# Kernel tuning notes

Hardware: AMD Instinct MI355X
Metric: run time of the kernel (lower is better)

## Reference

```python
import jax, jax.numpy as jnp
import numpy as np

B, N, D, H = 2, 2048, 1024, 16
DK = D // H


def setup_inputs() -> dict:
    key = jax.random.key(0)
    ks = jax.random.split(key, 8)
    s = 1.0 / np.sqrt(D)  # keep projection outputs O(1)
    return {
        "x": jax.random.normal(ks[0], (B, N, D), jnp.float32),
        "alpha": jax.random.uniform(ks[1], (B, N), jnp.float32, -1.0, 1.0),
        "bias": jax.random.normal(ks[2], (B, N, N), jnp.float32) * 0.1,
        "Wq": jax.random.normal(ks[3], (D, D), jnp.float32) * s,
        "bq": jnp.zeros((D,), jnp.float32),
        "Wk": jax.random.normal(ks[4], (D, D), jnp.float32) * s,
        "bk": jnp.zeros((D,), jnp.float32),
        "Wv": jax.random.normal(ks[5], (D, D), jnp.float32) * s,
        "bv": jnp.zeros((D,), jnp.float32),
        "Wo": jax.random.normal(ks[6], (D, D), jnp.float32) * s,
        "bo": jnp.zeros((D,), jnp.float32),
    }


def reference(x, alpha, bias, Wq, bq, Wk, bk, Wv, bv, Wo, bo):
    b, n, d = x.shape
    # projections -> (B, H, N, DK)
    def split_heads(t):
        return t.reshape(b, n, H, DK).transpose(0, 2, 1, 3)

    q = split_heads(x @ Wq + bq)
    k = split_heads(x @ Wk + bk)
    v = split_heads(x @ Wv + bv)

    # salience rescale of keys/values: (B,1,N,1)
    scale = 1.0 + alpha[:, None, :, None]
    k = k * scale
    v = v * scale

    logits = jnp.einsum("bhnd,bhmd->bhnm", q, k) / np.float32(np.sqrt(DK))
    logits = logits + bias[:, None, :, :]  # broadcast over heads
    attn = jax.nn.softmax(logits, axis=-1)

    y = jnp.einsum("bhnm,bhmd->bhnd", attn, v)
    y = y.transpose(0, 2, 1, 3).reshape(b, n, d)
    return y @ Wo + bo
```

## Files before the change

### kernel.cpp

```cpp
#include <hip/hip_runtime.h>

typedef __attribute__((ext_vector_type(8))) short bf16x8;
typedef __attribute__((ext_vector_type(4))) float f32x4;

#define LOG2E 1.4426950408889634f

static __device__ __forceinline__ unsigned short f2bf(float f) {
    unsigned int u = __builtin_bit_cast(unsigned int, f);
    u += 0x7fffu + ((u >> 16) & 1u);
    return (unsigned short)(u >> 16);
}
static __device__ __forceinline__ float bf2f(unsigned short h) {
    unsigned int u = ((unsigned int)h) << 16;
    return __builtin_bit_cast(float, u);
}
static __device__ __forceinline__ void gload_lds16(const void* g, void* l) {
    __builtin_amdgcn_global_load_lds(
        (const __attribute__((address_space(1))) void*)g,
        (__attribute__((address_space(3))) void*)l, 16, 0, 0);
}

__global__ void convert_bf16(const float* __restrict__ src,
                             unsigned short* __restrict__ dst, int n8) {
    int i = blockIdx.x * blockDim.x + threadIdx.x;
    if (i >= n8) return;
    const float4* s4 = (const float4*)src;
    float4 a = s4[2 * i], b = s4[2 * i + 1];
    uint4 u;
    u.x = (unsigned)f2bf(a.x) | ((unsigned)f2bf(a.y) << 16);
    u.y = (unsigned)f2bf(a.z) | ((unsigned)f2bf(a.w) << 16);
    u.z = (unsigned)f2bf(b.x) | ((unsigned)f2bf(b.y) << 16);
    u.w = (unsigned)f2bf(b.z) | ((unsigned)f2bf(b.w) << 16);
    *(uint4*)(dst + 8 * (size_t)i) = u;
}

__global__ void bias_permute(const float* __restrict__ src,
                             unsigned short* __restrict__ dst) {
    int mt = blockIdx.x, qt = blockIdx.y, b = blockIdx.z;
    int tid = threadIdx.x, w = tid >> 6, lane = tid & 63;
    int quad = lane >> 4, l16 = lane & 15;
    const float* s = src + (size_t)b * 2048 * 2048;
    unsigned short* d = dst + (((size_t)(b * 16 + qt) * 32 + mt) * 8192);
    for (int e = 0; e < 2; e++) {
        unsigned short vals[16];
        for (int c = 0; c < 4; c++)
            for (int r = 0; r < 4; r++) {
                int q = qt * 128 + e * 64 + w * 16 + quad * 4 + r;
                int k = mt * 64 + c * 16 + l16;
                vals[c * 4 + r] = f2bf(s[(size_t)q * 2048 + k] * LOG2E);
            }
        unsigned short* o = d + ((size_t)((e * 4 + w) * 64 + lane)) * 16;
        *(bf16x8*)&o[0] = *(bf16x8*)&vals[0];
        *(bf16x8*)&o[8] = *(bf16x8*)&vals[8];
    }
}

__global__ void transpose_convert4(const float* __restrict__ W0,
                                   const float* __restrict__ W1,
                                   const float* __restrict__ W2,
                                   const float* __restrict__ W3,
                                   unsigned short* __restrict__ T0,
                                   unsigned short* __restrict__ T1,
                                   unsigned short* __restrict__ T2,
                                   unsigned short* __restrict__ T3) {
    const float* W = (blockIdx.z == 0) ? W0 : (blockIdx.z == 1) ? W1
                     : (blockIdx.z == 2) ? W2 : W3;
    unsigned short* Wt = (blockIdx.z == 0) ? T0 : (blockIdx.z == 1) ? T1
                         : (blockIdx.z == 2) ? T2 : T3;
    __shared__ float t[32][33];
    int tx = threadIdx.x, ty = threadIdx.y;
    int x0 = blockIdx.x * 32, y0 = blockIdx.y * 32;
    for (int i = 0; i < 4; i++)
        t[ty + 8 * i][tx] = W[(size_t)(y0 + ty + 8 * i) * 1024 + x0 + tx];
    __syncthreads();
    for (int i = 0; i < 4; i++)
        Wt[(size_t)(x0 + ty + 8 * i) * 1024 + y0 + tx] = f2bf(t[tx][ty + 8 * i]);
}

__launch_bounds__(256)
__global__ void gemm_qkv(const unsigned short* __restrict__ A,
                         const unsigned short* __restrict__ WqT,
                         const unsigned short* __restrict__ WkT,
                         const unsigned short* __restrict__ WvT,
                         const float* __restrict__ bq,
                         const float* __restrict__ bk,
                         const float* __restrict__ bv,
                         const float* __restrict__ alpha,
                         unsigned short* __restrict__ Qb,
                         unsigned short* __restrict__ Kb,
                         unsigned short* __restrict__ Vtb) {
    int which = blockIdx.y >> 3;
    const unsigned short* Bt = (which == 0) ? WqT : (which == 1) ? WkT : WvT;
    const float* bias = (which == 0) ? bq : (which == 1) ? bk : bv;

    __shared__ __align__(16) unsigned short As[128][64];
    __shared__ __align__(16) unsigned short Bs[128][64];
    int tid = threadIdx.x;
    int wave = tid >> 6, lane = tid & 63, quad = lane >> 4, l16 = lane & 15;
    int wm = wave & 1, wn = wave >> 1;
    int lrow = lane >> 3, lblk = lane & 7;
    int swz = ((lblk ^ lrow) * 8);
    int m0 = blockIdx.x * 128, n0 = (blockIdx.y & 7) * 128;
    f32x4 acc[4][4] = {};

    for (int kt = 0; kt < 16; kt++) {
        int k0 = kt * 64;
        for (int i = 0; i < 4; i++) {
            int rbase = i * 32 + wave * 8;
            gload_lds16(&A[(size_t)(m0 + rbase + lrow) * 1024 + k0 + swz],
                        &As[rbase][0]);
            gload_lds16(&Bt[(size_t)(n0 + rbase + lrow) * 1024 + k0 + swz],
                        &Bs[rbase][0]);
        }
        __syncthreads();
        for (int ks = 0; ks < 2; ks++) {
            int pblk = ((ks * 4 + quad) ^ (l16 & 7)) * 8;
            bf16x8 af[4], bf_[4];
            for (int i = 0; i < 4; i++)
                af[i] = *(const bf16x8*)&As[64 * wm + 16 * i + l16][pblk];
            for (int j = 0; j < 4; j++)
                bf_[j] = *(const bf16x8*)&Bs[64 * wn + 16 * j + l16][pblk];
            if (which == 2) {
                for (int i = 0; i < 4; i++)
                    for (int j = 0; j < 4; j++)
                        acc[i][j] = __builtin_amdgcn_mfma_f32_16x16x32_bf16(
                            af[i], bf_[j], acc[i][j], 0, 0, 0);
            } else {
                for (int i = 0; i < 4; i++)
                    for (int j = 0; j < 4; j++)
                        acc[i][j] = __builtin_amdgcn_mfma_f32_16x16x32_bf16(
                            bf_[j], af[i], acc[i][j], 0, 0, 0);
            }
        }
        __syncthreads();
    }

    if (which == 2) {
        for (int i = 0; i < 4; i++)
            for (int j = 0; j < 4; j++) {
                int colb = n0 + 64 * wn + 16 * j + l16;
                int h = colb >> 6, dk = colb & 63;
                int row0 = m0 + 64 * wm + 16 * i + quad * 4;
                int bb = row0 >> 11, nn0 = row0 & 2047;
                unsigned short v4[4];
                for (int r = 0; r < 4; r++) {
                    float v = acc[i][j][r] + bias[colb];
                    v4[r] = f2bf(v * (1.0f + alpha[bb * 2048 + nn0 + r]));
                }
                uint2 u;
                u.x = (unsigned)v4[0] | ((unsigned)v4[1] << 16);
                u.y = (unsigned)v4[2] | ((unsigned)v4[3] << 16);
                *(uint2*)&Vtb[((size_t)(bb * 16 + h) * 64 + dk) * 2048 + nn0] = u;
            }
    } else {
        unsigned short* outb = (which == 0) ? Qb : Kb;
        for (int i = 0; i < 4; i++)
            for (int j = 0; j < 4; j++) {
                int row = m0 + 64 * wm + 16 * i + l16;
                int bb = row >> 11, nn = row & 2047;
                int colb0 = n0 + 64 * wn + 16 * j + quad * 4;
                int h = colb0 >> 6, dk0 = colb0 & 63;
                float4 b4 = *(const float4*)&bias[colb0];
                float s = (which == 0) ? (0.125f * LOG2E)
                                       : (1.0f + alpha[bb * 2048 + nn]);
                unsigned short v4[4];
                v4[0] = f2bf((acc[i][j][0] + b4.x) * s);
                v4[1] = f2bf((acc[i][j][1] + b4.y) * s);
                v4[2] = f2bf((acc[i][j][2] + b4.z) * s);
                v4[3] = f2bf((acc[i][j][3] + b4.w) * s);
                uint2 u;
                u.x = (unsigned)v4[0] | ((unsigned)v4[1] << 16);
                u.y = (unsigned)v4[2] | ((unsigned)v4[3] << 16);
                *(uint2*)&outb[((size_t)(bb * 16 + h) * 2048 + nn) * 64 + dk0] = u;
            }
    }
}

__launch_bounds__(256)
__global__ void gemm_out(const unsigned short* __restrict__ A,
                         const unsigned short* __restrict__ Bt,
                         const float* __restrict__ bias,
                         float* __restrict__ outf) {
    __shared__ __align__(16) unsigned short As[128][64];
    __shared__ __align__(16) unsigned short Bs[128][64];
    int tid = threadIdx.x;
    int wave = tid >> 6, lane = tid & 63, quad = lane >> 4, l16 = lane & 15;
    int wm = wave & 1, wn = wave >> 1;
    int lrow = lane >> 3, lblk = lane & 7;
    int swz = ((lblk ^ lrow) * 8);
    int m0 = blockIdx.x * 128, n0 = blockIdx.y * 128;
    f32x4 acc[4][4] = {};

    for (int kt = 0; kt < 16; kt++) {
        int k0 = kt * 64;
        for (int i = 0; i < 4; i++) {
            int rbase = i * 32 + wave * 8;
            gload_lds16(&A[(size_t)(m0 + rbase + lrow) * 1024 + k0 + swz],
                        &As[rbase][0]);
            gload_lds16(&Bt[(size_t)(n0 + rbase + lrow) * 1024 + k0 + swz],
                        &Bs[rbase][0]);
        }
        __syncthreads();
        for (int ks = 0; ks < 2; ks++) {
            int pblk = ((ks * 4 + quad) ^ (l16 & 7)) * 8;
            bf16x8 af[4], bf_[4];
            for (int i = 0; i < 4; i++)
                af[i] = *(const bf16x8*)&As[64 * wm + 16 * i + l16][pblk];
            for (int j = 0; j < 4; j++)
                bf_[j] = *(const bf16x8*)&Bs[64 * wn + 16 * j + l16][pblk];
            for (int i = 0; i < 4; i++)
                for (int j = 0; j < 4; j++)
                    acc[i][j] = __builtin_amdgcn_mfma_f32_16x16x32_bf16(
                        bf_[j], af[i], acc[i][j], 0, 0, 0);
        }
        __syncthreads();
    }

    for (int i = 0; i < 4; i++)
        for (int j = 0; j < 4; j++) {
            int row = m0 + 64 * wm + 16 * i + l16;
            int colb0 = n0 + 64 * wn + 16 * j + quad * 4;
            float4 b4 = *(const float4*)&bias[colb0];
            float4 o;
            o.x = acc[i][j][0] + b4.x;
            o.y = acc[i][j][1] + b4.y;
            o.z = acc[i][j][2] + b4.z;
            o.w = acc[i][j][3] + b4.w;
            *(float4*)&outf[(size_t)row * 1024 + colb0] = o;
        }
}

__launch_bounds__(256, 4)
__global__ void attn_kernel(const unsigned short* __restrict__ Q,
                            const unsigned short* __restrict__ K,
                            const unsigned short* __restrict__ Vt,
                            const unsigned short* __restrict__ biasP,
                            unsigned short* __restrict__ Y,
                            float* __restrict__ Opart,
                            float* __restrict__ Lpart, int split) {
    __shared__ __align__(16) unsigned short Ks[64][64];
    __shared__ __align__(16) unsigned short Vs[64][64];
    __shared__ __align__(16) unsigned short Ps[4][32][72];
    int tid = threadIdx.x;
    int wave = tid >> 6, lane = tid & 63, quad = lane >> 4, l16 = lane & 15;
    int qt = blockIdx.x, h = blockIdx.y;
    int b, mt0, mtN;
    if (split) { b = blockIdx.z >> 1; int half = blockIdx.z & 1;
                 mt0 = half * 16; mtN = mt0 + 16; }
    else       { b = blockIdx.z; mt0 = 0; mtN = 32; }
    int q0 = qt * 128;
    size_t headoff = (size_t)(b * 16 + h) * 2048 * 64;
    const unsigned short* Kp = K + headoff;
    const unsigned short* Vp = Vt + headoff;
    int lrow = lane >> 3, lblk = lane & 7;
    int swz = (lblk ^ lrow) * 8;

    bf16x8 aq[2][2];
    for (int e = 0; e < 2; e++) {
        const unsigned short* qp =
            Q + headoff + (size_t)(q0 + e * 64 + wave * 16 + l16) * 64;
        aq[e][0] = *(const bf16x8*)&qp[quad * 8];
        aq[e][1] = *(const bf16x8*)&qp[32 + quad * 8];
    }
    bf16x8 ones;
    for (int j = 0; j < 8; j++) ones[j] = (short)0x3F80;

    f32x4 oacc[2][4] = {};
    f32x4 lacc[2] = {};
    const unsigned short* bP = biasP + (size_t)(b * 16 + qt) * 32 * 8192;

    for (int mt = mt0; mt < mtN; mt++) {
        int m0 = mt * 64;
        for (int i = 0; i < 2; i++) {
            int rbase = wave * 16 + i * 8;
            gload_lds16(&Kp[(size_t)(m0 + rbase + lrow) * 64 + swz], &Ks[rbase][0]);
            gload_lds16(&Vp[(size_t)(rbase + lrow) * 2048 + m0 + swz], &Vs[rbase][0]);
        }
        const unsigned short* bt = bP + (size_t)mt * 8192;
        bf16x8 bz[2][2];
        for (int e = 0; e < 2; e++) {
            const unsigned short* p = bt + (size_t)((e * 4 + wave) * 64 + lane) * 16;
            bz[e][0] = *(const bf16x8*)&p[0];
            bz[e][1] = *(const bf16x8*)&p[8];
        }
        __syncthreads();

        f32x4 sc[2][4];
        for (int e = 0; e < 2; e++)
            for (int c = 0; c < 4; c++) {
                f32x4 s;
                for (int r = 0; r < 4; r++)
                    s[r] = bf2f(((unsigned short*)&bz[e][c >> 1])[(c & 1) * 4 + r]);
                sc[e][c] = s;
            }
        for (int c = 0; c < 4; c++) {
            for (int ks = 0; ks < 2; ks++) {
                bf16x8 kf = *(const bf16x8*)&Ks[c * 16 + l16]
                                               [((ks * 4 + quad) ^ (l16 & 7)) * 8];
                sc[0][c] = __builtin_amdgcn_mfma_f32_16x16x32_bf16(aq[0][ks], kf, sc[0][c], 0, 0, 0);
                sc[1][c] = __builtin_amdgcn_mfma_f32_16x16x32_bf16(aq[1][ks], kf, sc[1][c], 0, 0, 0);
            }
        }

        for (int e = 0; e < 2; e++)
            for (int c = 0; c < 4; c++) {
                int colw = (((c * 2 + (l16 >> 3)) + quad) & 7) * 8 + (l16 & 7);
                for (int r = 0; r < 4; r++) {
                    float p = exp2f(sc[e][c][r]);
                    unsigned int u = __builtin_bit_cast(unsigned int, p);
                    Ps[wave][e * 16 + quad * 4 + r][colw] = (unsigned short)(u >> 16);
                }
            }

        for (int ks = 0; ks < 2; ks++) {
            int blkr = (ks * 4 + quad + (l16 >> 2)) & 7;
            bf16x8 pf0 = *(const bf16x8*)&Ps[wave][l16][blkr * 8];
            bf16x8 pf1 = *(const bf16x8*)&Ps[wave][16 + l16][blkr * 8];
            lacc[0] = __builtin_amdgcn_mfma_f32_16x16x32_bf16(pf0, ones, lacc[0], 0, 0, 0);
            lacc[1] = __builtin_amdgcn_mfma_f32_16x16x32_bf16(pf1, ones, lacc[1], 0, 0, 0);
            for (int cv = 0; cv < 4; cv++) {
                bf16x8 vf = *(const bf16x8*)&Vs[cv * 16 + l16]
                                               [((ks * 4 + quad) ^ (l16 & 7)) * 8];
                oacc[0][cv] = __builtin_amdgcn_mfma_f32_16x16x32_bf16(pf0, vf, oacc[0][cv], 0, 0, 0);
                oacc[1][cv] = __builtin_amdgcn_mfma_f32_16x16x32_bf16(pf1, vf, oacc[1][cv], 0, 0, 0);
            }
        }
        __syncthreads();
    }

    if (split) {
        size_t p = ((size_t)((b * 16 + h) * 16 + qt)) * 2 + (blockIdx.z & 1);
        float* Op = Opart + p * 8192;
        for (int e = 0; e < 2; e++)
            for (int cv = 0; cv < 4; cv++)
                for (int r = 0; r < 4; r++)
                    Op[(e * 64 + wave * 16 + quad * 4 + r) * 64 + cv * 16 + l16] =
                        oacc[e][cv][r];
        if (l16 == 0)
            for (int e = 0; e < 2; e++)
                for (int r = 0; r < 4; r++)
                    Lpart[p * 128 + e * 64 + wave * 16 + quad * 4 + r] = lacc[e][r];
    } else {
        for (int e = 0; e < 2; e++) {
            float invl[4];
            for (int r = 0; r < 4; r++) invl[r] = 1.0f / lacc[e][r];
            for (int cv = 0; cv < 4; cv++)
                for (int r = 0; r < 4; r++) {
                    int qrow = q0 + e * 64 + 16 * wave + quad * 4 + r;
                    int d = h * 64 + cv * 16 + l16;
                    Y[((size_t)b * 2048 + qrow) * 1024 + d] =
                        f2bf(oacc[e][cv][r] * invl[r]);
                }
        }
    }
}

__global__ void attn_combine(const float* __restrict__ Opart,
                             const float* __restrict__ Lpart,
                             unsigned short* __restrict__ Y) {
    int blk = blockIdx.x;
    int qt = blk & 15, h = (blk >> 4) & 15, b = blk >> 8;
    const float* O0 = Opart + (size_t)blk * 2 * 8192;
    const float* O1 = O0 + 8192;
    const float* L0 = Lpart + (size_t)blk * 2 * 128;
    const float* L1 = L0 + 128;
    int t = threadIdx.x;
    for (int i = 0; i < 8; i++) {
        int idx4 = i * 256 + t;
        int q = idx4 >> 4;
        int dk = (idx4 & 15) * 4;
        float4 a = *(const float4*)&O0[idx4 * 4];
        float4 c = *(const float4*)&O1[idx4 * 4];
        float inv = 1.0f / (L0[q] + L1[q]);
        uint2 u;
        u.x = (unsigned)f2bf((a.x + c.x) * inv) |
              ((unsigned)f2bf((a.y + c.y) * inv) << 16);
        u.y = (unsigned)f2bf((a.z + c.z) * inv) |
              ((unsigned)f2bf((a.w + c.w) * inv) << 16);
        int qrow = qt * 128 + q;
        *(uint2*)&Y[((size_t)b * 2048 + qrow) * 1024 + h * 64 + dk] = u;
    }
}

extern "C" void kernel_launch(void* const* d_in, const int* in_sizes, int n_in,
                              void* d_out, int out_size, void* d_ws, size_t ws_size,
                              hipStream_t stream) {
    const float* x     = (const float*)d_in[0];
    const float* alpha = (const float*)d_in[1];
    const float* bias  = (const float*)d_in[2];
    const float* Wq    = (const float*)d_in[3];
    const float* bq    = (const float*)d_in[4];
    const float* Wk    = (const float*)d_in[5];
    const float* bk    = (const float*)d_in[6];
    const float* Wv    = (const float*)d_in[7];
    const float* bv    = (const float*)d_in[8];
    const float* Wo    = (const float*)d_in[9];
    const float* bo    = (const float*)d_in[10];
    float* out = (float*)d_out;

    char* ws = (char*)d_ws;
    const size_t MB = 1048576;
    unsigned short* xb    = (unsigned short*)(ws);
    unsigned short* wqt   = (unsigned short*)(ws + 8 * MB);
    unsigned short* wkt   = (unsigned short*)(ws + 10 * MB);
    unsigned short* wvt   = (unsigned short*)(ws + 12 * MB);
    unsigned short* wot   = (unsigned short*)(ws + 14 * MB);
    unsigned short* Qb    = (unsigned short*)(ws + 16 * MB);
    unsigned short* Kb    = (unsigned short*)(ws + 24 * MB);
    unsigned short* Vtb   = (unsigned short*)(ws + 32 * MB);
    unsigned short* biasP = (unsigned short*)(ws + 40 * MB);
    float*          Opart = (float*)(ws + 56 * MB);
    float*          Lpart = (float*)(ws + 88 * MB);
    unsigned short* Yb    = xb;
    int split = (ws_size >= 90 * MB) ? 1 : 0;

    convert_bf16<<<2048, 256, 0, stream>>>(x, xb, 524288);
    bias_permute<<<dim3(32, 16, 2), 256, 0, stream>>>(bias, biasP);
    transpose_convert4<<<dim3(32, 32, 4), dim3(32, 8), 0, stream>>>(
        Wq, Wk, Wv, Wo, wqt, wkt, wvt, wot);

    gemm_qkv<<<dim3(32, 24), 256, 0, stream>>>(
        xb, wqt, wkt, wvt, bq, bk, bv, alpha, Qb, Kb, Vtb);

    if (split) {
        attn_kernel<<<dim3(16, 16, 4), 256, 0, stream>>>(
            Qb, Kb, Vtb, biasP, Yb, Opart, Lpart, 1);
        attn_combine<<<512, 256, 0, stream>>>(Opart, Lpart, Yb);
    } else {
        attn_kernel<<<dim3(16, 16, 2), 256, 0, stream>>>(
            Qb, Kb, Vtb, biasP, Yb, Opart, Lpart, 0);
    }

    gemm_out<<<dim3(32, 8), 256, 0, stream>>>(Yb, wot, bo, out);
}
```

Measured before the change: 251.3 us.

## Merge prep kernels into one launch, stage bias through LDS, add MFMA priority hints

Replaces the three preprocessing launches (x conversion, weight transpose, bias permute) with a single prep kernel that dispatches on block index, removing two launch overheads. The bias permute now loads coalesced float4 rows into LDS before scattering, instead of strided global reads. In the attention loop, bias unpacking uses 32-bit word shifts and masks, and s_setprio raises wave priority around the MFMA sections. The merged kernel allocates 34KB of shared memory for every block, including x-conversion blocks that do not use it, which may lower occupancy for those blocks.

```diff
diff --git a/kernel.cpp b/kernel.cpp
--- a/kernel.cpp
+++ b/kernel.cpp
@@ -10,71 +10,80 @@
     u += 0x7fffu + ((u >> 16) & 1u);
     return (unsigned short)(u >> 16);
 }
-static __device__ __forceinline__ float bf2f(unsigned short h) {
-    unsigned int u = ((unsigned int)h) << 16;
-    return __builtin_bit_cast(float, u);
-}
 static __device__ __forceinline__ void gload_lds16(const void* g, void* l) {
     __builtin_amdgcn_global_load_lds(
         (const __attribute__((address_space(1))) void*)g,
         (__attribute__((address_space(3))) void*)l, 16, 0, 0);
 }
 
-__global__ void convert_bf16(const float* __restrict__ src,
-                             unsigned short* __restrict__ dst, int n8) {
-    int i = blockIdx.x * blockDim.x + threadIdx.x;
-    if (i >= n8) return;
-    const float4* s4 = (const float4*)src;
-    float4 a = s4[2 * i], b = s4[2 * i + 1];
-    uint4 u;
-    u.x = (unsigned)f2bf(a.x) | ((unsigned)f2bf(a.y) << 16);
-    u.y = (unsigned)f2bf(a.z) | ((unsigned)f2bf(a.w) << 16);
-    u.z = (unsigned)f2bf(b.x) | ((unsigned)f2bf(b.y) << 16);
-    u.w = (unsigned)f2bf(b.z) | ((unsigned)f2bf(b.w) << 16);
-    *(uint4*)(dst + 8 * (size_t)i) = u;
-}
-
-__global__ void bias_permute(const float* __restrict__ src,
-                             unsigned short* __restrict__ dst) {
-    int mt = blockIdx.x, qt = blockIdx.y, b = blockIdx.z;
-    int tid = threadIdx.x, w = tid >> 6, lane = tid & 63;
-    int quad = lane >> 4, l16 = lane & 15;
-    const float* s = src + (size_t)b * 2048 * 2048;
-    unsigned short* d = dst + (((size_t)(b * 16 + qt) * 32 + mt) * 8192);
-    for (int e = 0; e < 2; e++) {
-        unsigned short vals[16];
-        for (int c = 0; c < 4; c++)
-            for (int r = 0; r < 4; r++) {
-                int q = qt * 128 + e * 64 + w * 16 + quad * 4 + r;
-                int k = mt * 64 + c * 16 + l16;
-                vals[c * 4 + r] = f2bf(s[(size_t)q * 2048 + k] * LOG2E);
-            }
-        unsigned short* o = d + ((size_t)((e * 4 + w) * 64 + lane)) * 16;
-        *(bf16x8*)&o[0] = *(bf16x8*)&vals[0];
-        *(bf16x8*)&o[8] = *(bf16x8*)&vals[8];
-    }
-}
-
-__global__ void transpose_convert4(const float* __restrict__ W0,
-                                   const float* __restrict__ W1,
-                                   const float* __restrict__ W2,
-                                   const float* __restrict__ W3,
-                                   unsigned short* __restrict__ T0,
-                                   unsigned short* __restrict__ T1,
-                                   unsigned short* __restrict__ T2,
-                                   unsigned short* __restrict__ T3) {
-    const float* W = (blockIdx.z == 0) ? W0 : (blockIdx.z == 1) ? W1
-                     : (blockIdx.z == 2) ? W2 : W3;
-    unsigned short* Wt = (blockIdx.z == 0) ? T0 : (blockIdx.z == 1) ? T1
-                         : (blockIdx.z == 2) ? T2 : T3;
-    __shared__ float t[32][33];
-    int tx = threadIdx.x, ty = threadIdx.y;
-    int x0 = blockIdx.x * 32, y0 = blockIdx.y * 32;
-    for (int i = 0; i < 4; i++)
-        t[ty + 8 * i][tx] = W[(size_t)(y0 + ty + 8 * i) * 1024 + x0 + tx];
-    __syncthreads();
-    for (int i = 0; i < 4; i++)
-        Wt[(size_t)(x0 + ty + 8 * i) * 1024 + y0 + tx] = f2bf(t[tx][ty + 8 * i]);
+__launch_bounds__(256)
+__global__ void prep(const float* __restrict__ x,
+                     unsigned short* __restrict__ xb,
+                     const float* __restrict__ W0, const float* __restrict__ W1,
+                     const float* __restrict__ W2, const float* __restrict__ W3,
+                     unsigned short* __restrict__ T0, unsigned short* __restrict__ T1,
+                     unsigned short* __restrict__ T2, unsigned short* __restrict__ T3,
+                     const float* __restrict__ bias,
+                     unsigned short* __restrict__ biasP) {
+    __shared__ __align__(16) float smem[8704];
+    int id = blockIdx.x, tid = threadIdx.x;
+
+    if (id < 2048) {
+        int i = id * 256 + tid;
+        const float4* s4 = (const float4*)x;
+        float4 a = s4[2 * i], b = s4[2 * i + 1];
+        uint4 u;
+        u.x = (unsigned)f2bf(a.x) | ((unsigned)f2bf(a.y) << 16);
+        u.y = (unsigned)f2bf(a.z) | ((unsigned)f2bf(a.w) << 16);
+        u.z = (unsigned)f2bf(b.x) | ((unsigned)f2bf(b.y) << 16);
+        u.w = (unsigned)f2bf(b.z) | ((unsigned)f2bf(b.w) << 16);
+        *(uint4*)(xb + 8 * (size_t)i) = u;
+        return;
+    }
+    if (id < 6144) {
+        int j = id - 2048, which = j >> 10, r = j & 1023;
+        const float* W = (which == 0) ? W0 : (which == 1) ? W1
+                         : (which == 2) ? W2 : W3;
+        unsigned short* Wt = (which == 0) ? T0 : (which == 1) ? T1
+                             : (which == 2) ? T2 : T3;
+        int tx = tid & 31, ty = tid >> 5;
+        int x0 = (r & 31) * 32, y0 = (r >> 5) * 32;
+        float* t = smem;
+        for (int i = 0; i < 4; i++)
+            t[(ty + 8 * i) * 33 + tx] =
+                W[(size_t)(y0 + ty + 8 * i) * 1024 + x0 + tx];
+        __syncthreads();
+        for (int i = 0; i < 4; i++)
+            Wt[(size_t)(x0 + ty + 8 * i) * 1024 + y0 + tx] =
+                f2bf(t[tx * 33 + ty + 8 * i]);
+        return;
+    }
+    {
+        int j = id - 6144;
+        int mt = j & 31, qt = (j >> 5) & 15, b = j >> 9;
+        const float* s = bias + (size_t)b * 2048 * 2048;
+        float* Ls = smem;
+        for (int p = 0; p < 8; p++) {
+            int row = p * 16 + (tid >> 4), f4 = tid & 15;
+            float4 v = *(const float4*)
+                &s[(size_t)(qt * 128 + row) * 2048 + mt * 64 + f4 * 4];
+            *(float4*)&Ls[row * 68 + f4 * 4] = v;
+        }
+        __syncthreads();
+        int w = tid >> 6, lane = tid & 63, quad = lane >> 4, l16 = lane & 15;
+        unsigned short* d = biasP + (((size_t)(b * 16 + qt) * 32 + mt) * 8192);
+        for (int e = 0; e < 2; e++) {
+            unsigned short vals[16];
+            for (int c = 0; c < 4; c++)
+                for (int rr = 0; rr < 4; rr++)
+                    vals[c * 4 + rr] =
+                        f2bf(Ls[(e * 64 + w * 16 + quad * 4 + rr) * 68 +
+                                c * 16 + l16] * LOG2E);
+            unsigned short* o = d + ((size_t)((e * 4 + w) * 64 + lane)) * 16;
+            *(bf16x8*)&o[0] = *(bf16x8*)&vals[0];
+            *(bf16x8*)&o[8] = *(bf16x8*)&vals[8];
+        }
+    }
 }
 
 __launch_bounds__(256)
@@ -288,11 +297,15 @@
         f32x4 sc[2][4];
         for (int e = 0; e < 2; e++)
             for (int c = 0; c < 4; c++) {
+                uint2 w = ((const uint2*)&bz[e][c >> 1])[c & 1];
                 f32x4 s;
-                for (int r = 0; r < 4; r++)
-                    s[r] = bf2f(((unsigned short*)&bz[e][c >> 1])[(c & 1) * 4 + r]);
+                s[0] = __builtin_bit_cast(float, w.x << 16);
+                s[1] = __builtin_bit_cast(float, w.x & 0xffff0000u);
+                s[2] = __builtin_bit_cast(float, w.y << 16);
+                s[3] = __builtin_bit_cast(float, w.y & 0xffff0000u);
                 sc[e][c] = s;
             }
+        __builtin_amdgcn_s_setprio(1);
         for (int c = 0; c < 4; c++) {
             for (int ks = 0; ks < 2; ks++) {
                 bf16x8 kf = *(const bf16x8*)&Ks[c * 16 + l16]
@@ -301,6 +314,7 @@
                 sc[1][c] = __builtin_amdgcn_mfma_f32_16x16x32_bf16(aq[1][ks], kf, sc[1][c], 0, 0, 0);
             }
         }
+        __builtin_amdgcn_s_setprio(0);
 
         for (int e = 0; e < 2; e++)
             for (int c = 0; c < 4; c++) {
@@ -312,6 +326,7 @@
                 }
             }
 
+        __builtin_amdgcn_s_setprio(1);
         for (int ks = 0; ks < 2; ks++) {
             int blkr = (ks * 4 + quad + (l16 >> 2)) & 7;
             bf16x8 pf0 = *(const bf16x8*)&Ps[wave][l16][blkr * 8];
@@ -325,6 +340,7 @@
                 oacc[1][cv] = __builtin_amdgcn_mfma_f32_16x16x32_bf16(pf1, vf, oacc[1][cv], 0, 0, 0);
             }
         }
+        __builtin_amdgcn_s_setprio(0);
         __syncthreads();
     }
 
@@ -414,10 +430,8 @@
     unsigned short* Yb    = xb;
     int split = (ws_size >= 90 * MB) ? 1 : 0;
 
-    convert_bf16<<<2048, 256, 0, stream>>>(x, xb, 524288);
-    bias_permute<<<dim3(32, 16, 2), 256, 0, stream>>>(bias, biasP);
-    transpose_convert4<<<dim3(32, 32, 4), dim3(32, 8), 0, stream>>>(
-        Wq, Wk, Wv, Wo, wqt, wkt, wvt, wot);
+    prep<<<7168, 256, 0, stream>>>(x, xb, Wq, Wk, Wv, Wo,
+                                   wqt, wkt, wvt, wot, bias, biasP);
 
     gemm_qkv<<<dim3(32, 24), 256, 0, stream>>>(
         xb, wqt, wkt, wvt, bq, bk, bv, alpha, Qb, Kb, Vtb);
```

Result: faster. 244.0 us (-2.9%).
